# Kernel optimization log

Hardware: AMD Instinct MI355X
Metric: run time of the kernel (lower is better)

The kernel has to match this reference:

```python
import jax, jax.numpy as jnp
import numpy as np


def _normal_distance(n1, n2):
    # Cosine-style normal distance: 1 - <n1, n2>. The original module stubs
    # this as 0; we use the canonical mesh-normal loss so the cdist+argmin+
    # gather chain is exercised end-to-end.
    return 1.0 - jnp.sum(n1 * n2, axis=-1)


def setup_inputs() -> dict:
    key = jax.random.key(0)
    k1, k2, k3, k4 = jax.random.split(key, 4)
    N, M = 8192, 32768
    pred_pts = jax.random.normal(k1, (1, N, 3), dtype=jnp.float32)
    pred_nrm = jax.random.normal(k2, (1, N, 3), dtype=jnp.float32)
    gt_pts = jax.random.normal(k3, (1, M, 3), dtype=jnp.float32)
    gt_nrm = jax.random.normal(k4, (1, M, 3), dtype=jnp.float32)
    # unit normals, as on a real mesh
    pred_nrm = pred_nrm / jnp.linalg.norm(pred_nrm, axis=-1, keepdims=True)
    gt_nrm = gt_nrm / jnp.linalg.norm(gt_nrm, axis=-1, keepdims=True)
    return {
        "predicted_points_batch": pred_pts,
        "predicted_normals_batch": pred_nrm,
        "gt_points_batch": gt_pts,
        "gt_normals_batch": gt_nrm,
    }


def reference(predicted_points_batch, predicted_normals_batch,
              gt_points_batch, gt_normals_batch):
    # Original forward returns inside the first loop iteration -> element 0 only.
    p = predicted_points_batch[0]    # [N,3]
    pn = predicted_normals_batch[0]  # [N,3]
    g = gt_points_batch[0]           # [M,3]
    gn = gt_normals_batch[0]         # [M,3]

    # Squared pairwise distances (monotone in true cdist; only argmin is used).
    # d2[i,j] = |p_i|^2 + |g_j|^2 - 2 p_i . g_j   -> one [N,M] intermediate.
    d2 = (jnp.sum(p * p, axis=1)[:, None]
          + jnp.sum(g * g, axis=1)[None, :]
          - 2.0 * (p @ g.T))                      # [N,M]

    gt_idx = jnp.argmin(d2, axis=1)    # nearest gt point per predicted point, [N]
    pr_idx = jnp.argmin(d2, axis=0)    # nearest predicted point per gt point, [M]

    nearest_gt_normals = gn[gt_idx]    # [N,3]
    nearest_pr_normals = pn[pr_idx]    # [M,3]

    dist1 = _normal_distance(pn, nearest_gt_normals)  # [N]
    dist2 = _normal_distance(gn, nearest_pr_normals)  # [M]
    return jnp.mean(dist1) + jnp.mean(dist2)
```

## Files before the change

kernel.cpp:

```cpp
#include <hip/hip_runtime.h>
#include <stdint.h>
#include <float.h>

#define BLK 256
#define IPT 8
#define OWNERS (BLK * IPT)
#define SLICE 128
#define SUB 64

typedef unsigned long long ull;

__device__ __forceinline__ unsigned int ford(float f) {
    int b = __float_as_int(f);
    return (b >= 0) ? ((unsigned)b ^ 0x80000000u) : ~(unsigned)b;
}
__device__ __forceinline__ float ford_inv(unsigned int u) {
    int b = (u & 0x80000000u) ? (int)(u ^ 0x80000000u) : (int)~u;
    return __int_as_float(b);
}
__device__ __forceinline__ float vmin(float a, float b) {
    float d;
    asm("v_min_f32 %0, %1, %2" : "=v"(d) : "v"(a), "v"(b));
    return d;
}

__global__ __launch_bounds__(BLK) void nn_min_dual(
    const float* __restrict__ p, const float* __restrict__ g,
    ull* __restrict__ rowmin, ull* __restrict__ colmin,
    int rowBlocks, int rowSlices, int colSlices)
{
    __shared__ float4 sb[SLICE];

    const float* A; const float* B; ull* outmin; int id, nSlices;
    if ((int)blockIdx.x < rowBlocks) {
        id = blockIdx.x;             A = p; B = g; outmin = rowmin; nSlices = rowSlices;
    } else {
        id = blockIdx.x - rowBlocks; A = g; B = p; outmin = colmin; nSlices = colSlices;
    }
    const int chunk = id / nSlices;
    const int slice = id - chunk * nSlices;
    const int s0 = slice * SLICE;

    if (threadIdx.x < SLICE) {
        int s = s0 + threadIdx.x;
        float bx = B[3 * s], by = B[3 * s + 1], bz = B[3 * s + 2];
        float w = fmaf(bz, bz, fmaf(by, by, bx * bx));
        sb[threadIdx.x] = make_float4(bx, by, bz, w);
    }

    const int o0 = chunk * OWNERS + threadIdx.x;
    float ax[IPT], ay[IPT], az[IPT], best[IPT];
    int base[IPT];
#pragma unroll
    for (int r = 0; r < IPT; ++r) {
        int o = o0 + r * BLK;
        ax[r] = -2.0f * A[3 * o];
        ay[r] = -2.0f * A[3 * o + 1];
        az[r] = -2.0f * A[3 * o + 2];
        best[r] = FLT_MAX;
        base[r] = s0;
    }
    __syncthreads();

    for (int st = 0; st < SLICE; st += SUB) {
        float prev[IPT];
#pragma unroll
        for (int r = 0; r < IPT; ++r) prev[r] = best[r];

        float4 p0 = sb[st], p1 = sb[st + 1], p2 = sb[st + 2], p3 = sb[st + 3];
#pragma unroll 2
        for (int k = st; k < st + SUB; k += 4) {
            int kn = min(k + 4, SLICE - 4);
            float4 n0 = sb[kn], n1 = sb[kn + 1], n2 = sb[kn + 2], n3 = sb[kn + 3];
#pragma unroll
            for (int r = 0; r < IPT; ++r) {
                float v = fmaf(ax[r], p0.x, fmaf(ay[r], p0.y, fmaf(az[r], p0.z, p0.w)));
                best[r] = vmin(best[r], v);
            }
#pragma unroll
            for (int r = 0; r < IPT; ++r) {
                float v = fmaf(ax[r], p1.x, fmaf(ay[r], p1.y, fmaf(az[r], p1.z, p1.w)));
                best[r] = vmin(best[r], v);
            }
#pragma unroll
            for (int r = 0; r < IPT; ++r) {
                float v = fmaf(ax[r], p2.x, fmaf(ay[r], p2.y, fmaf(az[r], p2.z, p2.w)));
                best[r] = vmin(best[r], v);
            }
#pragma unroll
            for (int r = 0; r < IPT; ++r) {
                float v = fmaf(ax[r], p3.x, fmaf(ay[r], p3.y, fmaf(az[r], p3.z, p3.w)));
                best[r] = vmin(best[r], v);
            }
            p0 = n0; p1 = n1; p2 = n2; p3 = n3;
        }
#pragma unroll
        for (int r = 0; r < IPT; ++r)
            if (best[r] < prev[r]) base[r] = s0 + st;
    }

#pragma unroll
    for (int r = 0; r < IPT; ++r) {
        ull packed = ((ull)ford(best[r]) << 32) | (unsigned)base[r];
        atomicMax(&outmin[o0 + r * BLK], ~packed);
    }
}

__global__ __launch_bounds__(BLK) void finalize_kernel(
    const ull* __restrict__ rowmin, const ull* __restrict__ colmin,
    const float* __restrict__ p, const float* __restrict__ g,
    const float* __restrict__ pn, const float* __restrict__ gn,
    float* __restrict__ out, float* __restrict__ accum,
    unsigned int* __restrict__ done,
    int N, int M, float invN, float invM)
{
    const int lane = threadIdx.x & 63;
    const int wid  = (blockIdx.x * BLK + threadIdx.x) >> 6;
    const int nw   = (gridDim.x * BLK) >> 6;

    float wsum = 0.0f;
    for (int o = wid; o < N + M; o += nw) {
        const float* A; const float* B; const float* An; const float* Bn;
        ull stored; int oo; float inv;
        if (o < N) { oo = o;     A = p; B = g; An = pn; Bn = gn; stored = rowmin[oo]; inv = invN; }
        else       { oo = o - N; A = g; B = p; An = gn; Bn = pn; stored = colmin[oo]; inv = invM; }
        ull packed = ~stored;
        float bestv = ford_inv((unsigned int)(packed >> 32));
        int base = (int)(packed & 0xffffffffull);

        int s = base + lane;
        float bx = B[3 * s], by = B[3 * s + 1], bz = B[3 * s + 2];
        float w = fmaf(bz, bz, fmaf(by, by, bx * bx));
        float ax = -2.0f * A[3 * oo];
        float ay = -2.0f * A[3 * oo + 1];
        float az = -2.0f * A[3 * oo + 2];
        float v = fmaf(ax, bx, fmaf(ay, by, fmaf(az, bz, w)));

        ull mask = __ballot(v == bestv);
        int bit = mask ? (__ffsll(mask) - 1) : 0;
        int j = base + bit;

        if (lane == 0) {
            float d = An[3 * oo] * Bn[3 * j] + An[3 * oo + 1] * Bn[3 * j + 1]
                    + An[3 * oo + 2] * Bn[3 * j + 2];
            wsum += (1.0f - d) * inv;
        }
    }

    __shared__ float part[BLK / 64];
    if (lane == 0) part[threadIdx.x >> 6] = wsum;
    __syncthreads();
    if (threadIdx.x == 0) {
        float s = 0.0f;
#pragma unroll
        for (int w = 0; w < BLK / 64; ++w) s += part[w];
        atomicAdd(accum, s);
        __threadfence();
        unsigned int c = atomicAdd(done, 1u);
        if (c == gridDim.x - 1) {
            __threadfence();
            float tot = atomicAdd(accum, 0.0f);
            out[0] = tot;
        }
    }
}

extern "C" void kernel_launch(void* const* d_in, const int* in_sizes, int n_in,
                              void* d_out, int out_size, void* d_ws, size_t ws_size,
                              hipStream_t stream) {
    const float* p  = (const float*)d_in[0];
    const float* pn = (const float*)d_in[1];
    const float* g  = (const float*)d_in[2];
    const float* gn = (const float*)d_in[3];
    const int N = in_sizes[0] / 3;
    const int M = in_sizes[2] / 3;

    ull* rowmin = (ull*)d_ws;
    ull* colmin = rowmin + N;
    float* accum = (float*)(colmin + M);
    unsigned int* done = (unsigned int*)(accum + 1);
    float* out = (float*)d_out;

    hipMemsetAsync(d_ws, 0, (size_t)(N + M) * sizeof(ull) + 16, stream);

    const int rowSlices = M / SLICE;
    const int colSlices = N / SLICE;
    const int rowBlocks = (N / OWNERS) * rowSlices;
    const int colBlocks = (M / OWNERS) * colSlices;
    nn_min_dual<<<rowBlocks + colBlocks, BLK, 0, stream>>>(
        p, g, rowmin, colmin, rowBlocks, rowSlices, colSlices);

    finalize_kernel<<<640, BLK, 0, stream>>>(
        rowmin, colmin, p, g, pn, gn, out, accum, done, N, M, 1.0f / N, 1.0f / M);
}
```

Baseline: 133.2 us.

## Double per-thread owners, drop sub-slice index tracking, rescan full slice in finalize

```diff
diff --git a/kernel.cpp b/kernel.cpp
--- a/kernel.cpp
+++ b/kernel.cpp
@@ -3,10 +3,9 @@
 #include <float.h>
 
 #define BLK 256
-#define IPT 8
+#define IPT 16
 #define OWNERS (BLK * IPT)
 #define SLICE 128
-#define SUB 64
 
 typedef unsigned long long ull;
 
@@ -18,13 +17,8 @@
     int b = (u & 0x80000000u) ? (int)(u ^ 0x80000000u) : (int)~u;
     return __int_as_float(b);
 }
-__device__ __forceinline__ float vmin(float a, float b) {
-    float d;
-    asm("v_min_f32 %0, %1, %2" : "=v"(d) : "v"(a), "v"(b));
-    return d;
-}
 
-__global__ __launch_bounds__(BLK) void nn_min_dual(
+__global__ __launch_bounds__(BLK, 4) void nn_min_dual(
     const float* __restrict__ p, const float* __restrict__ g,
     ull* __restrict__ rowmin, ull* __restrict__ colmin,
     int rowBlocks, int rowSlices, int colSlices)
@@ -50,7 +44,6 @@
 
     const int o0 = chunk * OWNERS + threadIdx.x;
     float ax[IPT], ay[IPT], az[IPT], best[IPT];
-    int base[IPT];
 #pragma unroll
     for (int r = 0; r < IPT; ++r) {
         int o = o0 + r * BLK;
@@ -58,50 +51,22 @@
         ay[r] = -2.0f * A[3 * o + 1];
         az[r] = -2.0f * A[3 * o + 2];
         best[r] = FLT_MAX;
-        base[r] = s0;
     }
     __syncthreads();
 
-    for (int st = 0; st < SLICE; st += SUB) {
-        float prev[IPT];
+#pragma unroll 4
+    for (int k = 0; k < SLICE; ++k) {
+        float4 q = sb[k];
 #pragma unroll
-        for (int r = 0; r < IPT; ++r) prev[r] = best[r];
-
-        float4 p0 = sb[st], p1 = sb[st + 1], p2 = sb[st + 2], p3 = sb[st + 3];
-#pragma unroll 2
-        for (int k = st; k < st + SUB; k += 4) {
-            int kn = min(k + 4, SLICE - 4);
-            float4 n0 = sb[kn], n1 = sb[kn + 1], n2 = sb[kn + 2], n3 = sb[kn + 3];
-#pragma unroll
-            for (int r = 0; r < IPT; ++r) {
-                float v = fmaf(ax[r], p0.x, fmaf(ay[r], p0.y, fmaf(az[r], p0.z, p0.w)));
-                best[r] = vmin(best[r], v);
-            }
-#pragma unroll
-            for (int r = 0; r < IPT; ++r) {
-                float v = fmaf(ax[r], p1.x, fmaf(ay[r], p1.y, fmaf(az[r], p1.z, p1.w)));
-                best[r] = vmin(best[r], v);
-            }
-#pragma unroll
-            for (int r = 0; r < IPT; ++r) {
-                float v = fmaf(ax[r], p2.x, fmaf(ay[r], p2.y, fmaf(az[r], p2.z, p2.w)));
-                best[r] = vmin(best[r], v);
-            }
-#pragma unroll
-            for (int r = 0; r < IPT; ++r) {
-                float v = fmaf(ax[r], p3.x, fmaf(ay[r], p3.y, fmaf(az[r], p3.z, p3.w)));
-                best[r] = vmin(best[r], v);
-            }
-            p0 = n0; p1 = n1; p2 = n2; p3 = n3;
+        for (int r = 0; r < IPT; ++r) {
+            float v = fmaf(ax[r], q.x, fmaf(ay[r], q.y, fmaf(az[r], q.z, q.w)));
+            best[r] = fminf(best[r], v);
         }
-#pragma unroll
-        for (int r = 0; r < IPT; ++r)
-            if (best[r] < prev[r]) base[r] = s0 + st;
     }
 
 #pragma unroll
     for (int r = 0; r < IPT; ++r) {
-        ull packed = ((ull)ford(best[r]) << 32) | (unsigned)base[r];
+        ull packed = ((ull)ford(best[r]) << 32) | (unsigned)s0;
         atomicMax(&outmin[o0 + r * BLK], ~packed);
     }
 }
@@ -128,17 +93,24 @@
         float bestv = ford_inv((unsigned int)(packed >> 32));
         int base = (int)(packed & 0xffffffffull);
 
-        int s = base + lane;
-        float bx = B[3 * s], by = B[3 * s + 1], bz = B[3 * s + 2];
-        float w = fmaf(bz, bz, fmaf(by, by, bx * bx));
         float ax = -2.0f * A[3 * oo];
         float ay = -2.0f * A[3 * oo + 1];
         float az = -2.0f * A[3 * oo + 2];
-        float v = fmaf(ax, bx, fmaf(ay, by, fmaf(az, bz, w)));
 
-        ull mask = __ballot(v == bestv);
-        int bit = mask ? (__ffsll(mask) - 1) : 0;
-        int j = base + bit;
+        int s1 = base + lane;
+        float bx1 = B[3 * s1], by1 = B[3 * s1 + 1], bz1 = B[3 * s1 + 2];
+        int s2 = s1 + 64;
+        float bx2 = B[3 * s2], by2 = B[3 * s2 + 1], bz2 = B[3 * s2 + 2];
+
+        float w1 = fmaf(bz1, bz1, fmaf(by1, by1, bx1 * bx1));
+        float v1 = fmaf(ax, bx1, fmaf(ay, by1, fmaf(az, bz1, w1)));
+        float w2 = fmaf(bz2, bz2, fmaf(by2, by2, bx2 * bx2));
+        float v2 = fmaf(ax, bx2, fmaf(ay, by2, fmaf(az, bz2, w2)));
+
+        ull m1 = __ballot(v1 == bestv);
+        ull m2 = __ballot(v2 == bestv);
+        int j = m1 ? (base + __ffsll(m1) - 1)
+                   : (m2 ? (base + 64 + __ffsll(m2) - 1) : base);
 
         if (lane == 0) {
             float d = An[3 * oo] * Bn[3 * j] + An[3 * oo + 1] * Bn[3 * j + 1]
@@ -190,6 +162,6 @@
     nn_min_dual<<<rowBlocks + colBlocks, BLK, 0, stream>>>(
         p, g, rowmin, colmin, rowBlocks, rowSlices, colSlices);
 
-    finalize_kernel<<<640, BLK, 0, stream>>>(
+    finalize_kernel<<<1280, BLK, 0, stream>>>(
         rowmin, colmin, p, g, pn, gn, out, accum, done, N, M, 1.0f / N, 1.0f / M);
 }
```

After: 144.6 us. 8.6% more time.
